# Optimization experiments

Measured on AMD Instinct MI355X. Metric: run time of the kernel, lower is better.

## Reference

```python
import jax, jax.numpy as jnp
import numpy as np

WS, SS, IMG, NH = 7, 3, 56, 6  # window, shift, image size, heads
N = WS * WS                    # tokens per window = 49


def _rel_pos_index():
    coords = np.stack(np.meshgrid(np.arange(WS), np.arange(WS), indexing='ij')).reshape(2, -1)
    rel = (coords[:, :, None] - coords[:, None, :]).transpose(1, 2, 0)  # (N,N,2)
    rel[..., 0] += WS - 1
    rel[..., 1] += WS - 1
    rel[..., 0] *= 2 * WS - 1
    return rel.sum(-1)  # (N,N) int


def _attn_mask():
    m = np.zeros((IMG, IMG), np.float32)
    sl = (slice(0, -WS), slice(-WS, -SS), slice(-SS, None))
    cnt = 0
    for hs in sl:
        for ws_ in sl:
            m[hs, ws_] = cnt
            cnt += 1
    mw = m.reshape(IMG // WS, WS, IMG // WS, WS).transpose(0, 2, 1, 3).reshape(-1, N)  # (nW,N)
    diff = mw[:, None, :] - mw[:, :, None]
    return np.where(diff != 0, -100.0, 0.0).astype(np.float32)  # (nW,N,N)


def _ln(x, g, b, eps=1e-5):
    mu = x.mean(-1, keepdims=True)
    var = ((x - mu) ** 2).mean(-1, keepdims=True)
    return (x - mu) * jax.lax.rsqrt(var + eps) * g + b


def reference(x, rpb_table, w_qkv, b_qkv, w_proj, b_proj, g0, be0, g1, be1, w_fc1, b_fc1, w_fc2, b_fc2):
    B, C, _, _ = x.shape
    dh = C // NH
    nWs = IMG // WS
    nW = nWs * nWs

    xs = x.transpose(0, 2, 3, 1)            # NHWC [B,IMG,IMG,C]
    shortcut = xs
    h = _ln(xs, g0, be0)
    h = jnp.roll(h, (-SS, -SS), axis=(1, 2))
    # window partition -> [B*nW, N, C]
    h = h.reshape(B, nWs, WS, nWs, WS, C).transpose(0, 1, 3, 2, 4, 5).reshape(B * nW, N, C)

    qkv = h @ w_qkv.T + b_qkv               # [B_,N,3C]
    qkv = qkv.reshape(B * nW, N, dh, NH, 3)  # matches torch reshape (b_,N,C//h,h,3)
    q = qkv[..., 0].transpose(0, 3, 1, 2) * (dh ** -0.5)  # [B_,H,N,dh]
    k = qkv[..., 1].transpose(0, 3, 1, 2)
    v = qkv[..., 2].transpose(0, 3, 1, 2)

    att = jnp.einsum('bhnd,bhmd->bhnm', q, k)             # [B_,H,N,N]
    bias = rpb_table[jnp.asarray(_rel_pos_index().reshape(-1))].reshape(N, N, NH).transpose(2, 0, 1)
    att = att + bias[None]
    mask = jnp.asarray(_attn_mask())                      # [nW,N,N]
    att = att.reshape(B, nW, NH, N, N) + mask[None, :, None]
    att = jax.nn.softmax(att.reshape(B * nW, NH, N, N), axis=-1)

    o = jnp.einsum('bhnm,bhmd->bnhd', att, v).reshape(B * nW, WS, WS, C)
    o = o @ w_proj.T + b_proj
    # window reverse -> [B,IMG,IMG,C]
    o = o.reshape(B, nWs, nWs, WS, WS, C).transpose(0, 1, 3, 2, 4, 5).reshape(B, IMG, IMG, C)
    o = jnp.roll(o, (SS, SS), axis=(1, 2))

    xs = shortcut + o
    h2 = _ln(xs, g1, be1)
    h2 = jax.nn.gelu(h2 @ w_fc1.T + b_fc1, approximate=False) @ w_fc2.T + b_fc2
    xs = xs + h2
    return xs.transpose(0, 3, 1, 2)  # back to NCHW


def setup_inputs() -> dict:
    key = jax.random.key(0)
    ks = jax.random.split(key, 8)
    C, Hn = 192, 768
    return {
        'x': jax.random.normal(ks[0], (64, C, 56, 56), jnp.float32),
        'rpb_table': jax.random.normal(ks[1], (169, NH), jnp.float32) * 0.02,
        'w_qkv': jax.random.normal(ks[2], (3 * C, C), jnp.float32) * 0.02,
        'b_qkv': jnp.zeros((3 * C,), jnp.float32),
        'w_proj': jax.random.normal(ks[3], (C, C), jnp.float32) * 0.02,
        'b_proj': jnp.zeros((C,), jnp.float32),
        'g0': jnp.ones((C,), jnp.float32),
        'be0': jnp.zeros((C,), jnp.float32),
        'g1': jnp.ones((C,), jnp.float32),
        'be1': jnp.zeros((C,), jnp.float32),
        'w_fc1': jax.random.normal(ks[4], (Hn, C), jnp.float32) * 0.02,
        'b_fc1': jnp.zeros((Hn,), jnp.float32),
        'w_fc2': jax.random.normal(ks[5], (C, Hn), jnp.float32) * 0.02,
        'b_fc2': jnp.zeros((C,), jnp.float32),
    }
```

## Files before the change

kernel.cpp:

```cpp
#include <hip/hip_runtime.h>
#include <hip/hip_bf16.h>

typedef unsigned short ushortT;
typedef __attribute__((ext_vector_type(8))) short short8;
typedef __attribute__((ext_vector_type(4))) float f32x4;

#define MFMA16(a,b,c) __builtin_amdgcn_mfma_f32_16x16x32_bf16(a,b,c,0,0,0)

__device__ __forceinline__ ushortT f2bf(float f){
  union {float f; unsigned u;} v; v.f = f;
  unsigned r = v.u + 0x7FFFu + ((v.u >> 16) & 1u);
  return (ushortT)(r >> 16);
}
__device__ __forceinline__ float bf2f(ushortT u){
  union {unsigned u; float f;} v; v.u = ((unsigned)u) << 16; return v.f;
}
__device__ __forceinline__ float gelu_f(float v){
  float u = 0.7978845608028654f * (v + 0.044715f*v*v*v);
  float e = __expf(2.0f*u);
  return 0.5f * v * (1.0f + (1.0f - 2.0f/(e + 1.0f)));
}

#define SCALE_Q 0.17677669529663687f

__global__ void k_prep(const float* __restrict__ rpb, const float* __restrict__ wqkv,
                       const float* __restrict__ bqkv, const float* __restrict__ wproj,
                       const float* __restrict__ wfc1, const float* __restrict__ wfc2,
                       ushortT* __restrict__ wqkvp, float* __restrict__ bqkvp,
                       ushortT* __restrict__ wprojb, ushortT* __restrict__ wfc1b,
                       ushortT* __restrict__ wfc2b, float* __restrict__ bm)
{
  int i = blockIdx.x * 256 + threadIdx.x;
  if (i < 110592){
    int rp = i / 192, c = i % 192;
    int s = rp / 192, rem = rp % 192, hh = rem / 32, d = rem % 32;
    int rin = d*18 + hh*3 + s;
    float v = wqkv[rin*192 + c];
    if (s == 0) v *= SCALE_Q;
    wqkvp[i] = f2bf(v);
    return;
  }
  i -= 110592;
  if (i < 576){
    int rp = i;
    int s = rp / 192, rem = rp % 192, hh = rem / 32, d = rem % 32;
    int rin = d*18 + hh*3 + s;
    float v = bqkv[rin];
    if (s == 0) v *= SCALE_Q;
    bqkvp[i] = v;
    return;
  }
  i -= 576;
  if (i < 36864){ wprojb[i] = f2bf(wproj[i]); return; }
  i -= 36864;
  if (i < 147456){ wfc1b[i] = f2bf(wfc1[i]); return; }
  i -= 147456;
  if (i < 147456){ wfc2b[i] = f2bf(wfc2[i]); return; }
  i -= 147456;
  if (i < 921984){
    int j = i % 49; int t = i / 49; int ii = t % 49; t /= 49; int hh = t % 6; int w = t / 6;
    int r1 = ii/7, c1 = ii%7, r2 = j/7, c2 = j%7;
    int idx = (r1 - r2 + 6)*13 + (c1 - c2 + 6);
    float bias = rpb[idx*6 + hh];
    int wy = w >> 3, wx = w & 7;
    int hi = wy*7 + r1, wi = wx*7 + c1, hj = wy*7 + r2, wj = wx*7 + c2;
    int regi = 3*((hi<49)?0:((hi<53)?1:2)) + ((wi<49)?0:((wi<53)?1:2));
    int regj = 3*((hj<49)?0:((hj<53)?1:2)) + ((wj<49)?0:((wj<53)?1:2));
    bm[i] = bias + ((regi != regj) ? -100.0f : 0.0f);
  }
}

__global__ void k_tr(const float* __restrict__ x, ushortT* __restrict__ xsb)
{
  __shared__ float tile[192*57];
  int bh = blockIdx.x; int b = bh / 56, h = bh % 56;
  const float* src = x + (size_t)b*602112 + (size_t)h*56;
  for (int e = threadIdx.x; e < 192*56; e += 256){
    int c = e / 56, w = e % 56;
    tile[c*57 + w] = src[(size_t)c*3136 + w];
  }
  __syncthreads();
  ushortT* dst = xsb + (size_t)bh*56*192;
  for (int e = threadIdx.x; e < 56*192; e += 256){
    int w = e / 192, c = e % 192;
    dst[(size_t)w*192 + c] = f2bf(tile[c*57 + w]);
  }
}

__global__ __launch_bounds__(256,2) void k_attn(
  ushortT* __restrict__ xsb, const ushortT* __restrict__ wqkvp, const float* __restrict__ bqkvp,
  const ushortT* __restrict__ wprojb, const float* __restrict__ bproj,
  const float* __restrict__ g0, const float* __restrict__ be0,
  const float* __restrict__ g1, const float* __restrict__ be1,
  const float* __restrict__ bm, ushortT* __restrict__ xs2b)
{
  __shared__ ushortT ln0[49][200];
  __shared__ ushortT ks[49][200];
  __shared__ ushortT vT[6][32][72];
  __shared__ ushortT Pw[4][16][72];

  const int tid = threadIdx.x;
  const int lane = tid & 63, wv = tid >> 6;
  const int l15 = lane & 15, g = lane >> 4;
  const int wid = blockIdx.x;
  const int b = wid >> 6, wloc = wid & 63, wy = wloc >> 3, wx = wloc & 7;
  const int mbase = wv * 16;

  unsigned xr01[13]; ushortT xr2[13];
  #pragma unroll
  for (int it = 0; it < 13; it++){
    int t = wv + it*4;
    if (t < 49){
      int r = t / 7, cc = t % 7;
      int hsrc = (wy*7 + r + 3) % 56;
      int wsrc = (wx*7 + cc + 3) % 56;
      const ushortT* px = xsb + ((size_t)((b*56 + hsrc)*56 + wsrc))*192;
      ushortT r0 = px[lane], r1 = px[lane+64], r2 = px[lane+128];
      xr01[it] = ((unsigned)r1 << 16) | r0; xr2[it] = r2;
      float x0 = bf2f(r0), x1 = bf2f(r1), x2 = bf2f(r2);
      float s = x0 + x1 + x2, sq = x0*x0 + x1*x1 + x2*x2;
      #pragma unroll
      for (int m = 1; m < 64; m <<= 1){ s += __shfl_xor(s, m, 64); sq += __shfl_xor(sq, m, 64); }
      float mu = s * (1.0f/192.0f);
      float var = sq * (1.0f/192.0f) - mu*mu;
      float rs = rsqrtf(var + 1e-5f);
      ln0[t][lane]     = f2bf((x0-mu)*rs*g0[lane]     + be0[lane]);
      ln0[t][lane+64]  = f2bf((x1-mu)*rs*g0[lane+64]  + be0[lane+64]);
      ln0[t][lane+128] = f2bf((x2-mu)*rs*g0[lane+128] + be0[lane+128]);
    }
  }
  __syncthreads();

  {
    short8 a[4][6];
    #pragma unroll
    for (int mt = 0; mt < 4; mt++){
      int ra = mt*16 + l15; if (ra > 48) ra = 48;
      #pragma unroll
      for (int kc = 0; kc < 6; kc++)
        a[mt][kc] = *(const short8*)(&ln0[ra][kc*32 + g*8]);
    }
    __syncthreads();
    for (int ntl = 0; ntl < 9; ntl++){
      int nt = wv*9 + ntl;
      int cp = nt*16 + l15;
      const ushortT* wp = wqkvp + (size_t)cp*192 + g*8;
      short8 bfr[6];
      #pragma unroll
      for (int kc = 0; kc < 6; kc++) bfr[kc] = *(const short8*)(wp + kc*32);
      float bias = bqkvp[cp];
      #pragma unroll
      for (int mt = 0; mt < 4; mt++){
        f32x4 acc = {0.f,0.f,0.f,0.f};
        #pragma unroll
        for (int kc = 0; kc < 6; kc++) acc = MFMA16(a[mt][kc], bfr[kc], acc);
        #pragma unroll
        for (int r = 0; r < 4; r++){
          int tok = mt*16 + g*4 + r;
          float v = acc[r] + bias;
          if (cp < 192)      { if (tok < 49) ln0[tok][cp] = f2bf(v); }
          else if (cp < 384) { if (tok < 49) ks[tok][cp-192] = f2bf(v); }
          else { int c2 = cp - 384; vT[c2>>5][c2&31][tok] = f2bf(v); }
        }
      }
    }
  }
  __syncthreads();

  const int rq = (mbase + l15 > 48) ? 48 : (mbase + l15);
  for (int h = 0; h < 6; h++){
    float bmv[4][4];
    #pragma unroll
    for (int r = 0; r < 4; r++){
      int i = mbase + g*4 + r;
      int ic = (i < 49) ? i : 48;
      const float* bmrow = bm + (((size_t)(wloc*6 + h)*49 + ic)*49);
      #pragma unroll
      for (int jt = 0; jt < 4; jt++){
        int j = jt*16 + l15;
        bmv[r][jt] = (i < 49 && j < 49) ? bmrow[j] : -1e30f;
      }
    }
    short8 aq = *(const short8*)(&ln0[rq][h*32 + g*8]);
    f32x4 sreg[4];
    #pragma unroll
    for (int jt = 0; jt < 4; jt++){
      int rk = jt*16 + l15; if (rk > 48) rk = 48;
      short8 bk = *(const short8*)(&ks[rk][h*32 + g*8]);
      f32x4 z = {0.f,0.f,0.f,0.f};
      sreg[jt] = MFMA16(aq, bk, z);
    }
    #pragma unroll
    for (int r = 0; r < 4; r++){
      float rv[4];
      #pragma unroll
      for (int jt = 0; jt < 4; jt++){
        float bmvv = bmv[r][jt];
        rv[jt] = (bmvv < -1e29f) ? -1e30f : sreg[jt][r] + bmvv;
      }
      float mx = fmaxf(fmaxf(rv[0],rv[1]), fmaxf(rv[2],rv[3]));
      #pragma unroll
      for (int m = 1; m < 16; m <<= 1) mx = fmaxf(mx, __shfl_xor(mx, m, 64));
      float sum = 0.f;
      #pragma unroll
      for (int jt = 0; jt < 4; jt++){ rv[jt] = __expf(rv[jt] - mx); sum += rv[jt]; }
      #pragma unroll
      for (int m = 1; m < 16; m <<= 1) sum += __shfl_xor(sum, m, 64);
      float rden = 1.0f / sum;
      #pragma unroll
      for (int jt = 0; jt < 4; jt++)
        Pw[wv][g*4+r][jt*16 + l15] = f2bf(rv[jt] * rden);
    }
    #pragma unroll
    for (int nt2 = 0; nt2 < 2; nt2++){
      f32x4 oacc = {0.f,0.f,0.f,0.f};
      #pragma unroll
      for (int kk = 0; kk < 2; kk++){
        short8 ap = *(const short8*)(&Pw[wv][l15][kk*32 + g*8]);
        short8 bv = *(const short8*)(&vT[h][nt2*16 + l15][kk*32 + g*8]);
        oacc = MFMA16(ap, bv, oacc);
      }
      #pragma unroll
      for (int r = 0; r < 4; r++){
        int tok = mbase + g*4 + r;
        if (tok < 49) ln0[tok][h*32 + nt2*16 + l15] = f2bf(oacc[r]);
      }
    }
  }
  __syncthreads();

  {
    short8 a2[4][6];
    #pragma unroll
    for (int mt = 0; mt < 4; mt++){
      int ra = mt*16 + l15; if (ra > 48) ra = 48;
      #pragma unroll
      for (int kc = 0; kc < 6; kc++)
        a2[mt][kc] = *(const short8*)(&ln0[ra][kc*32 + g*8]);
    }
    __syncthreads();
    #pragma unroll
    for (int ntl = 0; ntl < 3; ntl++){
      int nt = wv*3 + ntl;
      int cp = nt*16 + l15;
      const ushortT* wp = wprojb + (size_t)cp*192 + g*8;
      short8 bfr[6];
      #pragma unroll
      for (int kc = 0; kc < 6; kc++) bfr[kc] = *(const short8*)(wp + kc*32);
      #pragma unroll
      for (int mt = 0; mt < 4; mt++){
        f32x4 acc = {0.f,0.f,0.f,0.f};
        #pragma unroll
        for (int kc = 0; kc < 6; kc++) acc = MFMA16(a2[mt][kc], bfr[kc], acc);
        #pragma unroll
        for (int r = 0; r < 4; r++){
          int tok = mt*16 + g*4 + r;
          if (tok < 49) ln0[tok][cp] = f2bf(acc[r]);
        }
      }
    }
  }
  __syncthreads();

  #pragma unroll
  for (int it = 0; it < 13; it++){
    int t = wv + it*4;
    if (t < 49){
      int rr = t / 7, cc = t % 7;
      int hdst = (wy*7 + rr + 3) % 56, wdst = (wx*7 + cc + 3) % 56;
      size_t gtok = ((size_t)(b*56 + hdst)*56 + wdst)*192;
      float v0 = bf2f(ln0[t][lane])     + bproj[lane]     + bf2f((ushortT)(xr01[it] & 0xFFFFu));
      float v1 = bf2f(ln0[t][lane+64])  + bproj[lane+64]  + bf2f((ushortT)(xr01[it] >> 16));
      float v2 = bf2f(ln0[t][lane+128]) + bproj[lane+128] + bf2f(xr2[it]);
      float s = v0 + v1 + v2, sq = v0*v0 + v1*v1 + v2*v2;
      #pragma unroll
      for (int m = 1; m < 64; m <<= 1){ s += __shfl_xor(s, m, 64); sq += __shfl_xor(sq, m, 64); }
      float mu = s * (1.0f/192.0f);
      float var = sq * (1.0f/192.0f) - mu*mu;
      float rs = rsqrtf(var + 1e-5f);
      xs2b[gtok + lane]     = f2bf(v0);
      xs2b[gtok + lane+64]  = f2bf(v1);
      xs2b[gtok + lane+128] = f2bf(v2);
      xsb[gtok + lane]     = f2bf((v0-mu)*rs*g1[lane]     + be1[lane]);
      xsb[gtok + lane+64]  = f2bf((v1-mu)*rs*g1[lane+64]  + be1[lane+64]);
      xsb[gtok + lane+128] = f2bf((v2-mu)*rs*g1[lane+128] + be1[lane+128]);
    }
  }
}

__global__ __launch_bounds__(512,4) void k_mlp_fused(
  const ushortT* __restrict__ A,
  const ushortT* __restrict__ w1g,
  const float* __restrict__ b1,
  const ushortT* __restrict__ w2g,
  const float* __restrict__ b2,
  const ushortT* __restrict__ xs2b,
  float* __restrict__ out)
{
  __shared__ ushortT w1s[12288];
  __shared__ ushortT w2s[12288];
  __shared__ ushortT Hbuf[128][72];
  const int tid = threadIdx.x, lane = tid & 63, wv = tid >> 6;
  const int l15 = lane & 15, g = lane >> 4;
  const size_t Mbase = (size_t)blockIdx.x * 128;
  const int rowb = wv * 16;

  short8 a[6];
  {
    size_t row = Mbase + rowb + l15;
    #pragma unroll
    for (int kc = 0; kc < 6; kc++)
      a[kc] = __builtin_nontemporal_load((const short8*)(A + row*192 + kc*32 + g*8));
  }

  short8 p1[3], p2[3];
  #define STAGE_LOAD(HB)                                                          \
    _Pragma("unroll")                                                             \
    for (int j = 0; j < 3; j++){                                                  \
      int u = j*512 + tid;                                                        \
      int hc = u & 63, cg = u >> 6;                                               \
      p1[j] = *(const short8*)(w1g + (size_t)((HB)*64 + hc)*192 + cg*8);          \
      int c2_ = u % 192, cc = u / 192;                                            \
      p2[j] = *(const short8*)(w2g + (size_t)c2_*768 + (HB)*64 + cc*8);           \
    }
  #define STAGE_WRITE()                                                           \
    _Pragma("unroll")                                                             \
    for (int j = 0; j < 3; j++){                                                  \
      int u = j*512 + tid;                                                        \
      int hc = u & 63, cg = u >> 6;                                               \
      int kc = cg >> 2, gq = cg & 3;                                              \
      int d1 = (((hc >> 4)*6 + kc)*4 + gq)*16 + (hc & 15);                        \
      *(short8*)(w1s + d1*8) = p1[j];                                             \
      int c2_ = u % 192, cc = u / 192;                                            \
      int kk = cc >> 2, gq2 = cc & 3;                                             \
      int d2 = (((c2_ >> 4)*2 + kk)*4 + gq2)*16 + (c2_ & 15);                     \
      *(short8*)(w2s + d2*8) = p2[j];                                             \
    }

  STAGE_LOAD(0);
  STAGE_WRITE();
  __syncthreads();

  f32x4 acc2[12];
  #pragma unroll
  for (int nt = 0; nt < 12; nt++) acc2[nt] = (f32x4){0.f,0.f,0.f,0.f};

  for (int hb = 0; hb < 12; hb++){
    if (hb < 11){ STAGE_LOAD(hb+1); }

    #pragma unroll
    for (int nt = 0; nt < 4; nt++){
      short8 bfr[6];
      #pragma unroll
      for (int kc = 0; kc < 6; kc++)
        bfr[kc] = *(const short8*)(w1s + ((((nt*6 + kc)*4 + g)*16 + l15))*8);
      float bias = b1[hb*64 + nt*16 + l15];
      f32x4 acc = {0.f,0.f,0.f,0.f};
      #pragma unroll
      for (int kc = 0; kc < 6; kc++) acc = MFMA16(a[kc], bfr[kc], acc);
      #pragma unroll
      for (int r = 0; r < 4; r++)
        Hbuf[rowb + g*4 + r][nt*16 + l15] = f2bf(gelu_f(acc[r] + bias));
    }
    short8 h2f[2];
    #pragma unroll
    for (int kk = 0; kk < 2; kk++)
      h2f[kk] = *(const short8*)(&Hbuf[rowb + l15][kk*32 + g*8]);
    #pragma unroll
    for (int nt = 0; nt < 12; nt++){
      short8 wfr[2];
      #pragma unroll
      for (int kk = 0; kk < 2; kk++)
        wfr[kk] = *(const short8*)(w2s + ((((nt*2 + kk)*4 + g)*16 + l15))*8);
      #pragma unroll
      for (int kk = 0; kk < 2; kk++)
        acc2[nt] = MFMA16(h2f[kk], wfr[kk], acc2[nt]);
    }
    if (hb < 11){
      __syncthreads();
      STAGE_WRITE();
      __syncthreads();
    }
  }

  #pragma unroll
  for (int nt = 0; nt < 12; nt++){
    int c = nt*16 + l15;
    float bs = b2[c];
    #pragma unroll
    for (int r = 0; r < 4; r++){
      size_t tok = Mbase + rowb + g*4 + r;
      float v = acc2[nt][r] + bs + bf2f(xs2b[tok*192 + c]);
      unsigned t32 = (unsigned)tok;
      unsigned bb = t32 / 3136u, rem = t32 % 3136u;
      out[(size_t)bb*602112 + (size_t)c*3136 + rem] = v;
    }
  }
  #undef STAGE_LOAD
  #undef STAGE_WRITE
}

extern "C" void kernel_launch(void* const* d_in, const int* in_sizes, int n_in,
                              void* d_out, int out_size, void* d_ws, size_t ws_size,
                              hipStream_t stream)
{
  const float* x      = (const float*)d_in[0];
  const float* rpb    = (const float*)d_in[1];
  const float* w_qkv  = (const float*)d_in[2];
  const float* b_qkv  = (const float*)d_in[3];
  const float* w_proj = (const float*)d_in[4];
  const float* b_proj = (const float*)d_in[5];
  const float* g0     = (const float*)d_in[6];
  const float* be0    = (const float*)d_in[7];
  const float* g1     = (const float*)d_in[8];
  const float* be1    = (const float*)d_in[9];
  const float* w_fc1  = (const float*)d_in[10];
  const float* b_fc1  = (const float*)d_in[11];
  const float* w_fc2  = (const float*)d_in[12];
  const float* b_fc2  = (const float*)d_in[13];
  float* out = (float*)d_out;
  char* ws = (char*)d_ws;

  ushortT* xsb    = (ushortT*)(ws);
  ushortT* xs2b   = (ushortT*)(ws + 77070336);
  ushortT* wqkvp  = (ushortT*)(ws + 154140672);
  float*   bqkvp  = (float*)(ws + 154361856);
  ushortT* wprojb = (ushortT*)(ws + 154364160);
  ushortT* wfc1b  = (ushortT*)(ws + 154437888);
  ushortT* wfc2b  = (ushortT*)(ws + 154732800);
  float*   bm     = (float*)(ws + 155027712);

  k_prep<<<5332, 256, 0, stream>>>(rpb, w_qkv, b_qkv, w_proj, w_fc1, w_fc2,
                                   wqkvp, bqkvp, wprojb, wfc1b, wfc2b, bm);
  k_tr<<<3584, 256, 0, stream>>>(x, xsb);
  k_attn<<<4096, 256, 0, stream>>>(xsb, wqkvp, bqkvp, wprojb, b_proj,
                                   g0, be0, g1, be1, bm, xs2b);
  k_mlp_fused<<<1568, 512, 0, stream>>>(xsb, wfc1b, b_fc1, wfc2b, b_fc2, xs2b, out);
}
```

Before: 825.4 us.

## Double-buffer MLP weight staging with direct global-to-LDS loads and half-size hidden chunks

```diff
diff --git a/kernel.cpp b/kernel.cpp
--- a/kernel.cpp
+++ b/kernel.cpp
@@ -4,6 +4,8 @@
 typedef unsigned short ushortT;
 typedef __attribute__((ext_vector_type(8))) short short8;
 typedef __attribute__((ext_vector_type(4))) float f32x4;
+typedef __attribute__((address_space(3))) unsigned int lds_uint;
+typedef __attribute__((address_space(1))) const unsigned int glob_uint;
 
 #define MFMA16(a,b,c) __builtin_amdgcn_mfma_f32_16x16x32_bf16(a,b,c,0,0,0)
 
@@ -297,9 +299,10 @@
   const ushortT* __restrict__ xs2b,
   float* __restrict__ out)
 {
-  __shared__ ushortT w1s[12288];
-  __shared__ ushortT w2s[12288];
-  __shared__ ushortT Hbuf[128][72];
+  __shared__ ushortT w1s[2][6144];
+  __shared__ ushortT w2s[2][6144];
+  __shared__ ushortT Hbuf[128][40];
+
   const int tid = threadIdx.x, lane = tid & 63, wv = tid >> 6;
   const int l15 = lane & 15, g = lane >> 4;
   const size_t Mbase = (size_t)blockIdx.x * 128;
@@ -313,48 +316,50 @@
       a[kc] = __builtin_nontemporal_load((const short8*)(A + row*192 + kc*32 + g*8));
   }
 
-  short8 p1[3], p2[3];
-  #define STAGE_LOAD(HB)                                                          \
-    _Pragma("unroll")                                                             \
-    for (int j = 0; j < 3; j++){                                                  \
-      int u = j*512 + tid;                                                        \
-      int hc = u & 63, cg = u >> 6;                                               \
-      p1[j] = *(const short8*)(w1g + (size_t)((HB)*64 + hc)*192 + cg*8);          \
-      int c2_ = u % 192, cc = u / 192;                                            \
-      p2[j] = *(const short8*)(w2g + (size_t)c2_*768 + (HB)*64 + cc*8);           \
-    }
-  #define STAGE_WRITE()                                                           \
-    _Pragma("unroll")                                                             \
-    for (int j = 0; j < 3; j++){                                                  \
-      int u = j*512 + tid;                                                        \
-      int hc = u & 63, cg = u >> 6;                                               \
-      int kc = cg >> 2, gq = cg & 3;                                              \
-      int d1 = (((hc >> 4)*6 + kc)*4 + gq)*16 + (hc & 15);                        \
-      *(short8*)(w1s + d1*8) = p1[j];                                             \
-      int c2_ = u % 192, cc = u / 192;                                            \
-      int kk = cc >> 2, gq2 = cc & 3;                                             \
-      int d2 = (((c2_ >> 4)*2 + kk)*4 + gq2)*16 + (c2_ & 15);                     \
-      *(short8*)(w2s + d2*8) = p2[j];                                             \
-    }
-
-  STAGE_LOAD(0);
-  STAGE_WRITE();
+  #define STAGE(HB, NB)                                                         \
+    _Pragma("unroll")                                                           \
+    for (int j = 0; j < 3; j++){                                                \
+      int id = wv + j*8;                                                        \
+      if (id < 12){                                                             \
+        int ci = id;                                                            \
+        int q = ci*4 + (lane >> 4);                                             \
+        int gq = q & 3, t = q >> 2;                                             \
+        int nt = t / 6, kc = t % 6;                                             \
+        const ushortT* src = w1g + (size_t)((HB)*32 + nt*16 + (lane & 15))*192  \
+                             + kc*32 + gq*8;                                    \
+        __builtin_amdgcn_global_load_lds((glob_uint*)src,                       \
+            (lds_uint*)(&w1s[NB][ci*512]), 16, 0, 0);                           \
+      } else {                                                                  \
+        int ci = id - 12;                                                       \
+        int q = ci*4 + (lane >> 4);                                             \
+        int nt = q >> 2, gq = q & 3;                                            \
+        const ushortT* src = w2g + (size_t)(nt*16 + (lane & 15))*768            \
+                             + (HB)*32 + gq*8;                                  \
+        __builtin_amdgcn_global_load_lds((glob_uint*)src,                       \
+            (lds_uint*)(&w2s[NB][ci*512]), 16, 0, 0);                           \
+      }                                                                         \
+    }
+
+  STAGE(0, 0);
   __syncthreads();
 
   f32x4 acc2[12];
   #pragma unroll
   for (int nt = 0; nt < 12; nt++) acc2[nt] = (f32x4){0.f,0.f,0.f,0.f};
 
-  for (int hb = 0; hb < 12; hb++){
-    if (hb < 11){ STAGE_LOAD(hb+1); }
-
-    #pragma unroll
-    for (int nt = 0; nt < 4; nt++){
+  for (int hb = 0; hb < 24; hb++){
+    const int cb = hb & 1;
+    if (hb < 23){ STAGE(hb+1, cb^1); }
+
+    #pragma unroll
+    for (int nt = 0; nt < 2; nt++){
       short8 bfr[6];
       #pragma unroll
-      for (int kc = 0; kc < 6; kc++)
-        bfr[kc] = *(const short8*)(w1s + ((((nt*6 + kc)*4 + g)*16 + l15))*8);
-      float bias = b1[hb*64 + nt*16 + l15];
+      for (int kc = 0; kc < 6; kc++){
+        int q = (nt*6 + kc)*4 + g;
+        bfr[kc] = *(const short8*)(&w1s[cb][(q*16 + l15)*8]);
+      }
+      float bias = b1[hb*32 + nt*16 + l15];
       f32x4 acc = {0.f,0.f,0.f,0.f};
       #pragma unroll
       for (int kc = 0; kc < 6; kc++) acc = MFMA16(a[kc], bfr[kc], acc);
@@ -362,25 +367,14 @@
       for (int r = 0; r < 4; r++)
         Hbuf[rowb + g*4 + r][nt*16 + l15] = f2bf(gelu_f(acc[r] + bias));
     }
-    short8 h2f[2];
-    #pragma unroll
-    for (int kk = 0; kk < 2; kk++)
-      h2f[kk] = *(const short8*)(&Hbuf[rowb + l15][kk*32 + g*8]);
+    short8 h2f = *(const short8*)(&Hbuf[rowb + l15][g*8]);
     #pragma unroll
     for (int nt = 0; nt < 12; nt++){
-      short8 wfr[2];
-      #pragma unroll
-      for (int kk = 0; kk < 2; kk++)
-        wfr[kk] = *(const short8*)(w2s + ((((nt*2 + kk)*4 + g)*16 + l15))*8);
-      #pragma unroll
-      for (int kk = 0; kk < 2; kk++)
-        acc2[nt] = MFMA16(h2f[kk], wfr[kk], acc2[nt]);
-    }
-    if (hb < 11){
-      __syncthreads();
-      STAGE_WRITE();
-      __syncthreads();
-    }
+      int q2 = nt*4 + g;
+      short8 wfr = *(const short8*)(&w2s[cb][(q2*16 + l15)*8]);
+      acc2[nt] = MFMA16(h2f, wfr, acc2[nt]);
+    }
+    __syncthreads();
   }
 
   #pragma unroll
@@ -396,8 +390,7 @@
       out[(size_t)bb*602112 + (size_t)c*3136 + rem] = v;
     }
   }
-  #undef STAGE_LOAD
-  #undef STAGE_WRITE
+  #undef STAGE
 }
 
 extern "C" void kernel_launch(void* const* d_in, const int* in_sizes, int n_in,
```

Measured after the change: 708.2 us. -14.2%, faster.
